# Kernel optimization log

Hardware: AMD Instinct MI355X
Metric: run time of the kernel (lower is better)

## Reference

```python
import jax, jax.numpy as jnp
import numpy as np

B, S, D_MODEL, D_K, D_V = 4, 2048, 1024, 64, 64


def setup_inputs() -> dict:
    key = jax.random.key(0)
    ks = jax.random.split(key, 6)
    Q = jax.random.normal(ks[0], (B, S, D_MODEL), dtype=jnp.float32)
    K = jax.random.normal(ks[1], (B, S, D_MODEL), dtype=jnp.float32)
    V = jax.random.normal(ks[2], (B, S, D_MODEL), dtype=jnp.float32)
    # Linear weights stored as [in, out] so projection is x @ W
    scale = 1.0 / np.sqrt(D_MODEL)
    WQ = jax.random.normal(ks[3], (D_MODEL, D_K), dtype=jnp.float32) * scale
    WK = jax.random.normal(ks[4], (D_MODEL, D_K), dtype=jnp.float32) * scale
    WV = jax.random.normal(ks[5], (D_MODEL, D_V), dtype=jnp.float32) * scale
    # causal mask: 1 = attend, 0 = masked (torch masked_fill(mask == 0, -inf))
    mask = jnp.tril(jnp.ones((S, S), dtype=jnp.int32))
    return {"Q": Q, "K": K, "V": V, "WQ": WQ, "WK": WK, "WV": WV, "mask": mask}


def reference(Q, K, V, WQ, WK, WV, mask):
    d_k = WQ.shape[-1]
    q = jnp.einsum("bsd,dk->bsk", Q, WQ)   # [B,S,d_k]
    k = jnp.einsum("bsd,dk->bsk", K, WK)   # [B,S,d_k]
    v = jnp.einsum("bsd,dv->bsv", V, WV)   # [B,S,d_v]
    scores = jnp.einsum("bqk,bsk->bqs", q, k) / jnp.sqrt(jnp.float32(d_k))
    scores = jnp.where(mask == 0, -jnp.inf, scores)  # broadcast [S,S] over batch
    attn = jax.nn.softmax(scores, axis=-1)
    H = jnp.einsum("bqs,bsv->bqv", attn, v)  # [B,S,d_v]
    return H
```

## Files before the change

### kernel.cpp

```cpp
#include <hip/hip_runtime.h>

typedef unsigned int u32;
typedef unsigned short u16;
using bf16x8 = __attribute__((ext_vector_type(8))) short;
using f32x4  = __attribute__((ext_vector_type(4))) float;

#define MFMA16 __builtin_amdgcn_mfma_f32_16x16x32_bf16

#define QH  (0u)
#define QL  (1u<<20)
#define KHO (2u<<20)
#define KLO (3u<<20)
#define VHO (4u<<20)
#define VLO (5u<<20)
#define VTH (6u<<20)
#define VTL (7u<<20)
#define WTH (8u<<20)
#define WTL (WTH + 3u*64*1024*2)
#define OPOFF (9u<<20)
#define PMOFF (OPOFF + 576u*4096*4)
#define PLOFF (PMOFF + 576u*64*4)

__device__ __forceinline__ u16 f2bf(float x) {
    u32 u = __float_as_uint(x);
    return (u16)((u + 0x7FFFu + ((u >> 16) & 1u)) >> 16);
}
__device__ __forceinline__ float bf2f(u16 h) {
    return __uint_as_float(((u32)h) << 16);
}

__device__ __forceinline__ int swz(int row, int c) {
    return c ^ ((row ^ (row >> 3)) & 7);
}
__device__ __forceinline__ bf16x8 ldsf(const char* t, int row, int c) {
    return *reinterpret_cast<const bf16x8*>(t + row * 128 + swz(row, c) * 16);
}
__device__ __forceinline__ void ldst(char* t, int row, int c, bf16x8 v) {
    *reinterpret_cast<bf16x8*>(t + row * 128 + swz(row, c) * 16) = v;
}

__device__ __forceinline__ void split8(float4 v0, float4 v1, bf16x8& h, bf16x8& l) {
    float e[8] = {v0.x, v0.y, v0.z, v0.w, v1.x, v1.y, v1.z, v1.w};
    #pragma unroll
    for (int j = 0; j < 8; ++j) {
        u16 hb = f2bf(e[j]);
        h[j] = (short)hb;
        l[j] = (short)f2bf(e[j] - bf2f(hb));
    }
}

__global__ __launch_bounds__(256) void wsplit_kernel(const float* __restrict__ WQ,
                                                     const float* __restrict__ WK,
                                                     const float* __restrict__ WV,
                                                     char* __restrict__ ws) {
    const int p = blockIdx.y, kt = blockIdx.x;
    const float* W = (p == 0) ? WQ : (p == 1) ? WK : WV;
    __shared__ float lds[64 * 68];
    const int t = threadIdx.x, row = t >> 2, cg = t & 3;
    const float* gp = W + ((size_t)kt * 64 + row) * 64 + cg * 16;
    #pragma unroll
    for (int j = 0; j < 16; ++j) lds[row * 68 + cg * 16 + j] = gp[j];
    __syncthreads();
    const int n = row, d0 = cg * 16;
    u32 wh[8], wl[8];
    #pragma unroll
    for (int j = 0; j < 8; ++j) {
        float x0 = lds[(d0 + 2 * j) * 68 + n];
        float x1 = lds[(d0 + 2 * j + 1) * 68 + n];
        u16 h0 = f2bf(x0), h1 = f2bf(x1);
        u16 l0 = f2bf(x0 - bf2f(h0)), l1 = f2bf(x1 - bf2f(h1));
        wh[j] = (u32)h0 | ((u32)h1 << 16);
        wl[j] = (u32)l0 | ((u32)l1 << 16);
    }
    u16* oh = (u16*)(ws + WTH) + (size_t)p * 64 * 1024 + (size_t)n * 1024 + kt * 64 + d0;
    u16* ol = (u16*)(ws + WTL) + (size_t)p * 64 * 1024 + (size_t)n * 1024 + kt * 64 + d0;
    uint4 a = {wh[0], wh[1], wh[2], wh[3]}, b = {wh[4], wh[5], wh[6], wh[7]};
    uint4 c = {wl[0], wl[1], wl[2], wl[3]}, d = {wl[4], wl[5], wl[6], wl[7]};
    *reinterpret_cast<uint4*>(oh) = a; *reinterpret_cast<uint4*>(oh + 8) = b;
    *reinterpret_cast<uint4*>(ol) = c; *reinterpret_cast<uint4*>(ol + 8) = d;
}

__global__ __launch_bounds__(256) void proj_kernel(const float* __restrict__ Q,
                                                   const float* __restrict__ K,
                                                   const float* __restrict__ V,
                                                   char* __restrict__ ws) {
    const int p = blockIdx.y;
    const float* X = (p == 0) ? Q : (p == 1) ? K : V;
    const u16* wth = (const u16*)(ws + WTH) + (size_t)p * 64 * 1024;
    const u16* wtl = (const u16*)(ws + WTL) + (size_t)p * 64 * 1024;
    u16* oh = (u16*)(ws + ((p == 0) ? QH : (p == 1) ? KHO : VHO));
    u16* ol = (u16*)(ws + ((p == 0) ? QL : (p == 1) ? KLO : VLO));
    const int rt = blockIdx.x;
    __shared__ char xh[8192], xl[8192], bh_[8192], bl_[8192];
    const int t = threadIdx.x, lane = t & 63, w = t >> 6;
    const int rs = t >> 2, cs = t & 3;

    auto ldrow = [&](int kc, float4* xr, bf16x8* wr) {
        const float* gp = X + (size_t)rt * 64 * 1024 + (size_t)rs * 1024 + kc + cs * 16;
        xr[0] = *reinterpret_cast<const float4*>(gp);
        xr[1] = *reinterpret_cast<const float4*>(gp + 4);
        xr[2] = *reinterpret_cast<const float4*>(gp + 8);
        xr[3] = *reinterpret_cast<const float4*>(gp + 12);
        const u16* ph_ = wth + (size_t)rs * 1024 + kc + cs * 16;
        const u16* pl_ = wtl + (size_t)rs * 1024 + kc + cs * 16;
        wr[0] = *reinterpret_cast<const bf16x8*>(ph_);
        wr[1] = *reinterpret_cast<const bf16x8*>(ph_ + 8);
        wr[2] = *reinterpret_cast<const bf16x8*>(pl_);
        wr[3] = *reinterpret_cast<const bf16x8*>(pl_ + 8);
    };

    f32x4 acc[4];
    #pragma unroll
    for (int nt = 0; nt < 4; ++nt) acc[nt] = (f32x4){0.f, 0.f, 0.f, 0.f};
    float4 xc[4], xn[4];
    bf16x8 wc[4], wn[4];
    ldrow(0, xc, wc);
    for (int kc = 0; kc < 1024; kc += 64) {
        __syncthreads();
        bf16x8 h0, l0, h1, l1;
        split8(xc[0], xc[1], h0, l0);
        split8(xc[2], xc[3], h1, l1);
        ldst(xh, rs, cs * 2, h0);     ldst(xl, rs, cs * 2, l0);
        ldst(xh, rs, cs * 2 + 1, h1); ldst(xl, rs, cs * 2 + 1, l1);
        ldst(bh_, rs, cs * 2, wc[0]); ldst(bh_, rs, cs * 2 + 1, wc[1]);
        ldst(bl_, rs, cs * 2, wc[2]); ldst(bl_, rs, cs * 2 + 1, wc[3]);
        if (kc + 64 < 1024) ldrow(kc + 64, xn, wn);
        __syncthreads();
        #pragma unroll
        for (int s = 0; s < 2; ++s) {
            bf16x8 ah = ldsf(xh, w * 16 + (lane & 15), s * 4 + (lane >> 4));
            bf16x8 al = ldsf(xl, w * 16 + (lane & 15), s * 4 + (lane >> 4));
            #pragma unroll
            for (int nt = 0; nt < 4; ++nt) {
                bf16x8 bh = ldsf(bh_, nt * 16 + (lane & 15), s * 4 + (lane >> 4));
                bf16x8 bl = ldsf(bl_, nt * 16 + (lane & 15), s * 4 + (lane >> 4));
                acc[nt] = MFMA16(ah, bh, acc[nt], 0, 0, 0);
                acc[nt] = MFMA16(ah, bl, acc[nt], 0, 0, 0);
                acc[nt] = MFMA16(al, bh, acc[nt], 0, 0, 0);
            }
        }
        #pragma unroll
        for (int i = 0; i < 4; ++i) { xc[i] = xn[i]; wc[i] = wn[i]; }
    }
    const float qs = (p == 0) ? 0.125f : 1.0f;
    #pragma unroll
    for (int nt = 0; nt < 4; ++nt)
        #pragma unroll
        for (int r = 0; r < 4; ++r) {
            float v = acc[nt][r] * qs;
            u16 hb = f2bf(v);
            u16 lb = f2bf(v - bf2f(hb));
            size_t idx = ((size_t)rt * 64 + w * 16 + (lane >> 4) * 4 + r) * 64 + nt * 16 + (lane & 15);
            oh[idx] = hb; ol[idx] = lb;
        }
}

__global__ __launch_bounds__(256) void vt_kernel(char* __restrict__ ws) {
    const int st = blockIdx.x, b = blockIdx.y;
    __shared__ u16 lh[64 * 72], ll[64 * 72];
    const int t = threadIdx.x, row = t >> 2, cg = t & 3;
    const u16* vh = (const u16*)(ws + VHO) + ((size_t)b * 2048 + st * 64 + row) * 64 + cg * 16;
    const u16* vl = (const u16*)(ws + VLO) + ((size_t)b * 2048 + st * 64 + row) * 64 + cg * 16;
    *reinterpret_cast<uint4*>(&lh[row * 72 + cg * 16]) = *reinterpret_cast<const uint4*>(vh);
    *reinterpret_cast<uint4*>(&lh[row * 72 + cg * 16 + 8]) = *reinterpret_cast<const uint4*>(vh + 8);
    *reinterpret_cast<uint4*>(&ll[row * 72 + cg * 16]) = *reinterpret_cast<const uint4*>(vl);
    *reinterpret_cast<uint4*>(&ll[row * 72 + cg * 16 + 8]) = *reinterpret_cast<const uint4*>(vl + 8);
    __syncthreads();
    const int d = row, s0 = cg * 16;
    u32 wh[8], wl[8];
    #pragma unroll
    for (int j = 0; j < 8; ++j) {
        wh[j] = (u32)lh[(s0 + 2 * j) * 72 + d] | ((u32)lh[(s0 + 2 * j + 1) * 72 + d] << 16);
        wl[j] = (u32)ll[(s0 + 2 * j) * 72 + d] | ((u32)ll[(s0 + 2 * j + 1) * 72 + d] << 16);
    }
    u16* th = (u16*)(ws + VTH) + ((size_t)b * 64 + d) * 2048 + st * 64 + s0;
    u16* tl = (u16*)(ws + VTL) + ((size_t)b * 64 + d) * 2048 + st * 64 + s0;
    uint4 a = {wh[0], wh[1], wh[2], wh[3]}, bb = {wh[4], wh[5], wh[6], wh[7]};
    uint4 c = {wl[0], wl[1], wl[2], wl[3]}, dd = {wl[4], wl[5], wl[6], wl[7]};
    *reinterpret_cast<uint4*>(th) = a; *reinterpret_cast<uint4*>(th + 8) = bb;
    *reinterpret_cast<uint4*>(tl) = c; *reinterpret_cast<uint4*>(tl + 8) = dd;
}

__device__ __forceinline__ int slot_base(int qt) {
    const int q4 = qt >> 2, r = qt & 3;
    return qt + 2 * q4 * (q4 - 1) + r * q4;
}

__global__ __launch_bounds__(256) void attn_kernel(char* __restrict__ ws) {
    const int chunk = blockIdx.x;
    const int qt = 31 - blockIdx.y;
    const int b = blockIdx.z;
    const int Li = qt + 1, kt0 = chunk * 4;
    if (kt0 >= Li) return;
    const int kt1 = (kt0 + 4 < Li) ? kt0 + 4 : Li;
    __shared__ char kh[8192], kl[8192], vh[8192], vl[8192], ph[8192], pl[8192];
    const int t = threadIdx.x, lane = t & 63, w = t >> 6;
    const int rs = t >> 2, cs = t & 3;
    const u16* qhg = (const u16*)(ws + QH);
    const u16* qlg = (const u16*)(ws + QL);
    const size_t qrow = (size_t)b * 2048 + qt * 64 + w * 16 + (lane & 15);
    bf16x8 qfh[2], qfl[2];
    #pragma unroll
    for (int s = 0; s < 2; ++s) {
        qfh[s] = *reinterpret_cast<const bf16x8*>(qhg + qrow * 64 + s * 32 + (lane >> 4) * 8);
        qfl[s] = *reinterpret_cast<const bf16x8*>(qlg + qrow * 64 + s * 32 + (lane >> 4) * 8);
    }
    const u16* kgh = (const u16*)(ws + KHO) + (size_t)b * 2048 * 64;
    const u16* kgl = (const u16*)(ws + KLO) + (size_t)b * 2048 * 64;
    const u16* vgh = (const u16*)(ws + VTH) + (size_t)b * 64 * 2048;
    const u16* vgl = (const u16*)(ws + VTL) + (size_t)b * 64 * 2048;

    auto ldreg = [&](int kt, bf16x8* r) {
        const u16* pk_h = kgh + (size_t)kt * 4096 + (size_t)rs * 64 + cs * 16;
        const u16* pk_l = kgl + (size_t)kt * 4096 + (size_t)rs * 64 + cs * 16;
        const u16* pv_h = vgh + (size_t)rs * 2048 + kt * 64 + cs * 16;
        const u16* pv_l = vgl + (size_t)rs * 2048 + kt * 64 + cs * 16;
        r[0] = *reinterpret_cast<const bf16x8*>(pk_h);
        r[1] = *reinterpret_cast<const bf16x8*>(pk_h + 8);
        r[2] = *reinterpret_cast<const bf16x8*>(pk_l);
        r[3] = *reinterpret_cast<const bf16x8*>(pk_l + 8);
        r[4] = *reinterpret_cast<const bf16x8*>(pv_h);
        r[5] = *reinterpret_cast<const bf16x8*>(pv_h + 8);
        r[6] = *reinterpret_cast<const bf16x8*>(pv_l);
        r[7] = *reinterpret_cast<const bf16x8*>(pv_l + 8);
    };
    auto stlds = [&](bf16x8* r) {
        ldst(kh, rs, cs * 2, r[0]); ldst(kh, rs, cs * 2 + 1, r[1]);
        ldst(kl, rs, cs * 2, r[2]); ldst(kl, rs, cs * 2 + 1, r[3]);
        ldst(vh, rs, cs * 2, r[4]); ldst(vh, rs, cs * 2 + 1, r[5]);
        ldst(vl, rs, cs * 2, r[6]); ldst(vl, rs, cs * 2 + 1, r[7]);
    };

    f32x4 o[4];
    #pragma unroll
    for (int nt = 0; nt < 4; ++nt) o[nt] = (f32x4){0.f, 0.f, 0.f, 0.f};
    float mrow[4], lrow[4];
    #pragma unroll
    for (int r = 0; r < 4; ++r) { mrow[r] = -1e30f; lrow[r] = 0.f; }

    bf16x8 rc[8], rn[8];
    ldreg(kt0, rc);
    for (int kt = kt0; kt < kt1; ++kt) {
        __syncthreads();
        stlds(rc);
        if (kt + 1 < kt1) ldreg(kt + 1, rn);
        __syncthreads();
        f32x4 sacc[4];
        #pragma unroll
        for (int nt = 0; nt < 4; ++nt) sacc[nt] = (f32x4){0.f, 0.f, 0.f, 0.f};
        #pragma unroll
        for (int s = 0; s < 2; ++s) {
            #pragma unroll
            for (int nt = 0; nt < 4; ++nt) {
                bf16x8 bh = ldsf(kh, nt * 16 + (lane & 15), s * 4 + (lane >> 4));
                bf16x8 bl = ldsf(kl, nt * 16 + (lane & 15), s * 4 + (lane >> 4));
                sacc[nt] = MFMA16(qfh[s], bh, sacc[nt], 0, 0, 0);
                sacc[nt] = MFMA16(qfh[s], bl, sacc[nt], 0, 0, 0);
                sacc[nt] = MFMA16(qfl[s], bh, sacc[nt], 0, 0, 0);
            }
        }
        if (kt == qt) {
            #pragma unroll
            for (int nt = 0; nt < 4; ++nt)
                #pragma unroll
                for (int r = 0; r < 4; ++r)
                    if (nt * 16 + (lane & 15) > w * 16 + (lane >> 4) * 4 + r)
                        sacc[nt][r] = -1e30f;
        }
        float pcur[4][4], scv[4];
        #pragma unroll
        for (int r = 0; r < 4; ++r) {
            float mx = fmaxf(fmaxf(sacc[0][r], sacc[1][r]), fmaxf(sacc[2][r], sacc[3][r]));
            #pragma unroll
            for (int off = 1; off < 16; off <<= 1) mx = fmaxf(mx, __shfl_xor(mx, off));
            const float nm = fmaxf(mrow[r], mx);
            scv[r] = __expf(mrow[r] - nm);
            mrow[r] = nm;
            float rs_ = 0.f;
            #pragma unroll
            for (int nt = 0; nt < 4; ++nt) {
                float pv = __expf(sacc[nt][r] - nm);
                pcur[nt][r] = pv; rs_ += pv;
            }
            #pragma unroll
            for (int off = 1; off < 16; off <<= 1) rs_ += __shfl_xor(rs_, off);
            lrow[r] = lrow[r] * scv[r] + rs_;
        }
        f32x4 scq = {scv[0], scv[1], scv[2], scv[3]};
        #pragma unroll
        for (int nt = 0; nt < 4; ++nt) o[nt] *= scq;
        #pragma unroll
        for (int nt = 0; nt < 4; ++nt)
            #pragma unroll
            for (int r = 0; r < 4; ++r) {
                const int row = w * 16 + (lane >> 4) * 4 + r;
                const int key = nt * 16 + (lane & 15);
                u16 hb = f2bf(pcur[nt][r]);
                u16 lb = f2bf(pcur[nt][r] - bf2f(hb));
                const int byt = row * 128 + swz(row, key >> 3) * 16 + (key & 7) * 2;
                *reinterpret_cast<u16*>(ph + byt) = hb;
                *reinterpret_cast<u16*>(pl + byt) = lb;
            }
        #pragma unroll
        for (int s = 0; s < 2; ++s) {
            bf16x8 pah = ldsf(ph, w * 16 + (lane & 15), s * 4 + (lane >> 4));
            bf16x8 pal = ldsf(pl, w * 16 + (lane & 15), s * 4 + (lane >> 4));
            #pragma unroll
            for (int nt = 0; nt < 4; ++nt) {
                bf16x8 vbh = ldsf(vh, nt * 16 + (lane & 15), s * 4 + (lane >> 4));
                bf16x8 vbl = ldsf(vl, nt * 16 + (lane & 15), s * 4 + (lane >> 4));
                o[nt] = MFMA16(pah, vbh, o[nt], 0, 0, 0);
                o[nt] = MFMA16(pah, vbl, o[nt], 0, 0, 0);
                o[nt] = MFMA16(pal, vbh, o[nt], 0, 0, 0);
            }
        }
        #pragma unroll
        for (int i = 0; i < 8; ++i) rc[i] = rn[i];
    }
    const int slot = b * 144 + slot_base(qt) + chunk;
    float* Op = (float*)(ws + OPOFF) + (size_t)slot * 4096;
    #pragma unroll
    for (int nt = 0; nt < 4; ++nt)
        #pragma unroll
        for (int r = 0; r < 4; ++r)
            Op[(size_t)(w * 16 + (lane >> 4) * 4 + r) * 64 + nt * 16 + (lane & 15)] = o[nt][r];
    if ((lane & 15) == 0) {
        float* Pm = (float*)(ws + PMOFF);
        float* Pl = (float*)(ws + PLOFF);
        #pragma unroll
        for (int r = 0; r < 4; ++r) {
            Pm[(size_t)slot * 64 + w * 16 + (lane >> 4) * 4 + r] = mrow[r];
            Pl[(size_t)slot * 64 + w * 16 + (lane >> 4) * 4 + r] = lrow[r];
        }
    }
}

__global__ __launch_bounds__(256) void merge_kernel(const char* __restrict__ ws,
                                                    float* __restrict__ out) {
    const int qt = blockIdx.x >> 4, rb = blockIdx.x & 15, b = blockIdx.y;
    const int t = threadIdx.x, d = t & 63, rloc = t >> 6;
    const int row = rb * 4 + rloc;
    const int Ci = (qt >> 2) + 1;
    const int slot0 = b * 144 + slot_base(qt);
    const float* Op = (const float*)(ws + OPOFF);
    const float* Pm = (const float*)(ws + PMOFF);
    const float* Pl = (const float*)(ws + PLOFF);
    float M = -1e30f;
    for (int c = 0; c < Ci; ++c) M = fmaxf(M, Pm[(size_t)(slot0 + c) * 64 + row]);
    float den = 0.f, acc = 0.f;
    for (int c = 0; c < Ci; ++c) {
        const float wv = __expf(Pm[(size_t)(slot0 + c) * 64 + row] - M);
        den += wv * Pl[(size_t)(slot0 + c) * 64 + row];
        acc += wv * Op[(size_t)(slot0 + c) * 4096 + (size_t)row * 64 + d];
    }
    out[(size_t)((b * 32 + qt) * 64 + row) * 64 + d] = acc / den;
}

extern "C" void kernel_launch(void* const* d_in, const int* in_sizes, int n_in,
                              void* d_out, int out_size, void* d_ws, size_t ws_size,
                              hipStream_t stream) {
    (void)in_sizes; (void)n_in; (void)out_size; (void)ws_size;
    const float* Q  = (const float*)d_in[0];
    const float* K  = (const float*)d_in[1];
    const float* V  = (const float*)d_in[2];
    const float* WQ = (const float*)d_in[3];
    const float* WK = (const float*)d_in[4];
    const float* WV = (const float*)d_in[5];
    char* ws   = (char*)d_ws;
    float* out = (float*)d_out;

    wsplit_kernel<<<dim3(16, 3), dim3(256), 0, stream>>>(WQ, WK, WV, ws);
    proj_kernel<<<dim3(128, 3), dim3(256), 0, stream>>>(Q, K, V, ws);
    vt_kernel<<<dim3(32, 4), dim3(256), 0, stream>>>(ws);
    attn_kernel<<<dim3(8, 32, 4), dim3(256), 0, stream>>>(ws);
    merge_kernel<<<dim3(512, 4), dim3(256), 0, stream>>>(ws, out);
}
```

Before: 191.4 us.

## Split projection K dimension across two blocks and read weights directly from global

The projection kernel now splits the 1024-wide reduction into two halves via blockIdx.z, doubling the grid from 384 to 768 blocks so more of the GPU's compute units are busy. Each half writes fp32 partial sums to a new workspace region, and a new combine kernel adds them, applies the Q scale and produces the hi/lo bf16 split. The weight operands are no longer staged in LDS. Each lane loads them straight from global memory (L2/L1-cached) inside the MFMA loop, which removes LDS traffic but may add load latency on the critical path. The change also adds an extra kernel launch and an fp32 partial round trip through memory.

```diff
diff --git a/kernel.cpp b/kernel.cpp
--- a/kernel.cpp
+++ b/kernel.cpp
@@ -20,6 +20,7 @@
 #define OPOFF (9u<<20)
 #define PMOFF (OPOFF + 576u*4096*4)
 #define PLOFF (PMOFF + 576u*64*4)
+#define PART  (32u<<20)
 
 __device__ __forceinline__ u16 f2bf(float x) {
     u32 u = __float_as_uint(x);
@@ -84,75 +85,83 @@
                                                    const float* __restrict__ K,
                                                    const float* __restrict__ V,
                                                    char* __restrict__ ws) {
-    const int p = blockIdx.y;
+    const int p = blockIdx.y, z = blockIdx.z;
     const float* X = (p == 0) ? Q : (p == 1) ? K : V;
     const u16* wth = (const u16*)(ws + WTH) + (size_t)p * 64 * 1024;
     const u16* wtl = (const u16*)(ws + WTL) + (size_t)p * 64 * 1024;
-    u16* oh = (u16*)(ws + ((p == 0) ? QH : (p == 1) ? KHO : VHO));
-    u16* ol = (u16*)(ws + ((p == 0) ? QL : (p == 1) ? KLO : VLO));
+    float* part = (float*)(ws + PART) + (size_t)(p * 2 + z) * 8192 * 64;
     const int rt = blockIdx.x;
-    __shared__ char xh[8192], xl[8192], bh_[8192], bl_[8192];
+    __shared__ char xh[8192], xl[8192];
     const int t = threadIdx.x, lane = t & 63, w = t >> 6;
     const int rs = t >> 2, cs = t & 3;
 
-    auto ldrow = [&](int kc, float4* xr, bf16x8* wr) {
+    auto ldrow = [&](int kc, float4* xr) {
         const float* gp = X + (size_t)rt * 64 * 1024 + (size_t)rs * 1024 + kc + cs * 16;
         xr[0] = *reinterpret_cast<const float4*>(gp);
         xr[1] = *reinterpret_cast<const float4*>(gp + 4);
         xr[2] = *reinterpret_cast<const float4*>(gp + 8);
         xr[3] = *reinterpret_cast<const float4*>(gp + 12);
-        const u16* ph_ = wth + (size_t)rs * 1024 + kc + cs * 16;
-        const u16* pl_ = wtl + (size_t)rs * 1024 + kc + cs * 16;
-        wr[0] = *reinterpret_cast<const bf16x8*>(ph_);
-        wr[1] = *reinterpret_cast<const bf16x8*>(ph_ + 8);
-        wr[2] = *reinterpret_cast<const bf16x8*>(pl_);
-        wr[3] = *reinterpret_cast<const bf16x8*>(pl_ + 8);
     };
 
     f32x4 acc[4];
     #pragma unroll
     for (int nt = 0; nt < 4; ++nt) acc[nt] = (f32x4){0.f, 0.f, 0.f, 0.f};
+    const int kc0 = z * 512, kc1 = kc0 + 512;
     float4 xc[4], xn[4];
-    bf16x8 wc[4], wn[4];
-    ldrow(0, xc, wc);
-    for (int kc = 0; kc < 1024; kc += 64) {
+    ldrow(kc0, xc);
+    for (int kc = kc0; kc < kc1; kc += 64) {
         __syncthreads();
         bf16x8 h0, l0, h1, l1;
         split8(xc[0], xc[1], h0, l0);
         split8(xc[2], xc[3], h1, l1);
         ldst(xh, rs, cs * 2, h0);     ldst(xl, rs, cs * 2, l0);
         ldst(xh, rs, cs * 2 + 1, h1); ldst(xl, rs, cs * 2 + 1, l1);
-        ldst(bh_, rs, cs * 2, wc[0]); ldst(bh_, rs, cs * 2 + 1, wc[1]);
-        ldst(bl_, rs, cs * 2, wc[2]); ldst(bl_, rs, cs * 2 + 1, wc[3]);
-        if (kc + 64 < 1024) ldrow(kc + 64, xn, wn);
+        if (kc + 64 < kc1) ldrow(kc + 64, xn);
         __syncthreads();
         #pragma unroll
         for (int s = 0; s < 2; ++s) {
             bf16x8 ah = ldsf(xh, w * 16 + (lane & 15), s * 4 + (lane >> 4));
             bf16x8 al = ldsf(xl, w * 16 + (lane & 15), s * 4 + (lane >> 4));
+            const u16* wbh = wth + (size_t)(lane & 15) * 1024 + kc + s * 32 + (lane >> 4) * 8;
+            const u16* wbl = wtl + (size_t)(lane & 15) * 1024 + kc + s * 32 + (lane >> 4) * 8;
             #pragma unroll
             for (int nt = 0; nt < 4; ++nt) {
-                bf16x8 bh = ldsf(bh_, nt * 16 + (lane & 15), s * 4 + (lane >> 4));
-                bf16x8 bl = ldsf(bl_, nt * 16 + (lane & 15), s * 4 + (lane >> 4));
+                bf16x8 bh = *reinterpret_cast<const bf16x8*>(wbh + (size_t)nt * 16 * 1024);
+                bf16x8 bl = *reinterpret_cast<const bf16x8*>(wbl + (size_t)nt * 16 * 1024);
                 acc[nt] = MFMA16(ah, bh, acc[nt], 0, 0, 0);
                 acc[nt] = MFMA16(ah, bl, acc[nt], 0, 0, 0);
                 acc[nt] = MFMA16(al, bh, acc[nt], 0, 0, 0);
             }
         }
         #pragma unroll
-        for (int i = 0; i < 4; ++i) { xc[i] = xn[i]; wc[i] = wn[i]; }
-    }
+        for (int i = 0; i < 4; ++i) xc[i] = xn[i];
+    }
+    #pragma unroll
+    for (int nt = 0; nt < 4; ++nt)
+        #pragma unroll
+        for (int r = 0; r < 4; ++r)
+            part[(size_t)(rt * 64 + w * 16 + (lane >> 4) * 4 + r) * 64 + nt * 16 + (lane & 15)] = acc[nt][r];
+}
+
+__global__ __launch_bounds__(256) void combine_kernel(char* __restrict__ ws) {
+    const int p = blockIdx.y;
+    const float* p0 = (const float*)(ws + PART) + (size_t)(p * 2) * 524288;
+    const float* p1 = p0 + 524288;
+    u16* oh = (u16*)(ws + ((p == 0) ? QH : (p == 1) ? KHO : VHO));
+    u16* ol = (u16*)(ws + ((p == 0) ? QL : (p == 1) ? KLO : VLO));
     const float qs = (p == 0) ? 0.125f : 1.0f;
-    #pragma unroll
-    for (int nt = 0; nt < 4; ++nt)
-        #pragma unroll
-        for (int r = 0; r < 4; ++r) {
-            float v = acc[nt][r] * qs;
-            u16 hb = f2bf(v);
-            u16 lb = f2bf(v - bf2f(hb));
-            size_t idx = ((size_t)rt * 64 + w * 16 + (lane >> 4) * 4 + r) * 64 + nt * 16 + (lane & 15);
-            oh[idx] = hb; ol[idx] = lb;
-        }
+    const size_t i0 = ((size_t)blockIdx.x * 256 + threadIdx.x) * 4;
+    float4 a = *reinterpret_cast<const float4*>(p0 + i0);
+    float4 b = *reinterpret_cast<const float4*>(p1 + i0);
+    float e[4] = {(a.x + b.x) * qs, (a.y + b.y) * qs, (a.z + b.z) * qs, (a.w + b.w) * qs};
+    ushort4 h, l;
+    u16 hb;
+    hb = f2bf(e[0]); h.x = hb; l.x = f2bf(e[0] - bf2f(hb));
+    hb = f2bf(e[1]); h.y = hb; l.y = f2bf(e[1] - bf2f(hb));
+    hb = f2bf(e[2]); h.z = hb; l.z = f2bf(e[2] - bf2f(hb));
+    hb = f2bf(e[3]); h.w = hb; l.w = f2bf(e[3] - bf2f(hb));
+    *reinterpret_cast<ushort4*>(oh + i0) = h;
+    *reinterpret_cast<ushort4*>(ol + i0) = l;
 }
 
 __global__ __launch_bounds__(256) void vt_kernel(char* __restrict__ ws) {
@@ -370,7 +379,8 @@
     float* out = (float*)d_out;
 
     wsplit_kernel<<<dim3(16, 3), dim3(256), 0, stream>>>(WQ, WK, WV, ws);
-    proj_kernel<<<dim3(128, 3), dim3(256), 0, stream>>>(Q, K, V, ws);
+    proj_kernel<<<dim3(128, 3, 2), dim3(256), 0, stream>>>(Q, K, V, ws);
+    combine_kernel<<<dim3(512, 3), dim3(256), 0, stream>>>(ws);
     vt_kernel<<<dim3(32, 4), dim3(256), 0, stream>>>(ws);
     attn_kernel<<<dim3(8, 32, 4), dim3(256), 0, stream>>>(ws);
     merge_kernel<<<dim3(512, 4), dim3(256), 0, stream>>>(ws, out);
```

Measured after the change: 223.8 us. +16.9%, slower.
